# Kernel optimization log

Hardware: AMD Instinct MI355X
Metric: run time of the kernel (lower is better)

Reference implementation:

```python
import jax, jax.numpy as jnp
import numpy as np

C_Z = 128
C_S = 1024
C_S_OUT = 1024
B, L = 1, 1024


def setup_inputs() -> dict:
    key = jax.random.key(0)
    ks = jax.random.split(key, 8)
    s_z = jax.random.normal(ks[0], (B, L, L, C_Z), dtype=jnp.float32)
    s_s_in = jax.random.normal(ks[1], (B, L, C_S), dtype=jnp.float32)
    pair_mask = jnp.ones((B, L, L), dtype=jnp.float32)
    scale = 0.02
    return {
        "s_z": s_z,
        "s_s_in": s_s_in,
        "pair_mask": pair_mask,
        "ln_g": jnp.ones((C_Z,), jnp.float32),
        "ln_b": jnp.zeros((C_Z,), jnp.float32),
        "w1": jax.random.normal(ks[2], (C_Z, C_Z), jnp.float32) * scale,
        "b1": jnp.zeros((C_Z,), jnp.float32),
        "w2": jax.random.normal(ks[3], (C_Z, C_Z), jnp.float32) * scale,
        "b2": jnp.zeros((C_Z,), jnp.float32),
        "wc": jax.random.normal(ks[4], (C_S_OUT, 2 * C_Z + C_S), jnp.float32) * scale,
        "bc": jnp.zeros((C_S_OUT,), jnp.float32),
    }


def _layernorm(x, g, b, eps=1e-5):
    mu = jnp.mean(x, axis=-1, keepdims=True)
    var = jnp.mean(jnp.square(x - mu), axis=-1, keepdims=True)
    return (x - mu) * jax.lax.rsqrt(var + eps) * g + b


def reference(s_z, s_s_in, pair_mask, ln_g, ln_b, w1, b1, w2, b2, wc, bc):
    # LayerNorm -> Linear -> ReLU -> Linear over last dim (c_z)
    z = _layernorm(s_z, ln_g, ln_b)
    z = jax.nn.relu(jnp.einsum("blmc,dc->blmd", z, w1) + b1)
    z = jnp.einsum("blmc,dc->blmd", z, w2) + b2
    z = z * pair_mask[..., None]
    # masked mean over columns (dim=2) and rows (dim=1)
    norm_c = jnp.clip(jnp.sum(pair_mask, axis=2), 1.0, None)  # (B, L)
    s_s_c = jnp.sum(z, axis=2) / norm_c[..., None]            # (B, L, c_z)
    norm_r = jnp.clip(jnp.sum(pair_mask, axis=1), 1.0, None)
    s_s_r = jnp.sum(z, axis=1) / norm_r[..., None]
    cat = jnp.concatenate([s_s_c, s_s_r, s_s_in], axis=-1)    # (B, L, 2*c_z + c_s)
    return jnp.einsum("blc,dc->bld", cat, wc) + bc            # (B, L, c_s_out)
```

## Files before the change

### kernel.cpp

```cpp
#include <hip/hip_runtime.h>
#include <hip/hip_bf16.h>


typedef short bf16x8 __attribute__((ext_vector_type(8)));
typedef short short4v __attribute__((ext_vector_type(4)));
typedef float f32x16 __attribute__((ext_vector_type(16)));

static __device__ __forceinline__ short f2bf(float f) {
  unsigned u = __float_as_uint(f);
  u += 0x7fffu + ((u >> 16) & 1u);
  return (short)(u >> 16);
}
static __device__ __forceinline__ float bf2f(short s) {
  return __uint_as_float(((unsigned)(unsigned short)s) << 16);
}

__global__ __launch_bounds__(512, 4) void k_pair(
    const float* __restrict__ z, const float* __restrict__ pm,
    const float* __restrict__ lng, const float* __restrict__ lnb,
    const float* __restrict__ w1, const float* __restrict__ b1,
    float* __restrict__ gP, float* __restrict__ grP,
    float* __restrict__ Mc, float* __restrict__ Mr)
{
  __shared__ __align__(16) short As[2][64 * 136];
  __shared__ __align__(16) float rowdat[2][64][4];

  const int tid  = threadIdx.x;
  const int lane = tid & 63;
  const int wv   = tid >> 6;
  const int rt   = wv >> 2;
  const int cq   = wv & 3;
  const int ln   = lane & 31;
  const int hh   = lane >> 5;
  const int bx   = blockIdx.x, by = blockIdx.y;
  const int l0   = by * 32;
  const int m0   = bx * 32;
  const int c8   = (tid & 15) * 8;
  const int rstage = tid >> 4;

  const int dcol = cq * 32 + ln;
  float uacc = 0.f, wacc = 0.f;
  bf16x8 bF[8];
  #pragma unroll
  for (int k0 = 0; k0 < 8; ++k0) {
    const int kb = k0 * 16 + hh * 8;
    const float* wp = w1 + dcol * 128 + kb;
    float4 f0 = *(const float4*)wp;
    float4 f1 = *(const float4*)(wp + 4);
    float4 g0 = *(const float4*)(lng + kb);
    float4 g1 = *(const float4*)(lng + kb + 4);
    float4 e0 = *(const float4*)(lnb + kb);
    float4 e1 = *(const float4*)(lnb + kb + 4);
    float wr[8] = {f0.x, f0.y, f0.z, f0.w, f1.x, f1.y, f1.z, f1.w};
    float gg[8] = {g0.x, g0.y, g0.z, g0.w, g1.x, g1.y, g1.z, g1.w};
    float be[8] = {e0.x, e0.y, e0.z, e0.w, e1.x, e1.y, e1.z, e1.w};
    bf16x8 t;
    #pragma unroll
    for (int j = 0; j < 8; ++j) {
      t[j] = f2bf(wr[j] * gg[j]);
      uacc += bf2f(t[j]);
      wacc += wr[j] * be[j];
    }
    bF[k0] = t;
  }
  uacc += __shfl_xor(uacc, 32);
  wacc += __shfl_xor(wacc, 32);
  const float u_d  = uacc;
  const float wb_d = wacc + b1[dcol];

  float grA[16];
  #pragma unroll
  for (int i = 0; i < 16; ++i) grA[i] = 0.f;
  float mrAcc = 0.f;

  float4 xa[2], xb[2];
  float  mv = 0.f;
  auto LOADB = [&](int b) {
    #pragma unroll
    for (int p = 0; p < 2; ++p) {
      const int r = p * 32 + rstage;
      const int l = l0 + b * 2 + (r >> 5);
      const int m = m0 + (r & 31);
      const float* src = z + ((size_t)l * 1024 + (size_t)m) * 128 + c8;
      xa[p] = *(const float4*)src;
      xb[p] = *(const float4*)(src + 4);
    }
    if (tid < 64)
      mv = pm[(size_t)(l0 + b * 2 + (tid >> 5)) * 1024 + (m0 + (tid & 31))];
  };

  LOADB(0);

  #pragma unroll 1
  for (int b = 0; b < 16; ++b) {
    const int buf = b & 1;
    #pragma unroll
    for (int p = 0; p < 2; ++p) {
      const int r = p * 32 + rstage;
      float x[8] = {xa[p].x, xa[p].y, xa[p].z, xa[p].w,
                    xb[p].x, xb[p].y, xb[p].z, xb[p].w};
      float s = 0.f, s2 = 0.f;
      #pragma unroll
      for (int j = 0; j < 8; ++j) { s += x[j]; s2 = fmaf(x[j], x[j], s2); }
      #pragma unroll
      for (int off = 1; off < 16; off <<= 1) {
        s  += __shfl_xor(s, off);
        s2 += __shfl_xor(s2, off);
      }
      const float mu  = s * (1.f / 128.f);
      const float var = s2 * (1.f / 128.f) - mu * mu;
      const float rs  = rsqrtf(var + 1e-5f);
      bf16x8 o;
      #pragma unroll
      for (int j = 0; j < 8; ++j) o[j] = f2bf(x[j]);
      *(bf16x8*)(&As[buf][r * 136 + c8]) = o;
      if ((tid & 15) == 0) {
        rowdat[buf][r][0] = rs;
        rowdat[buf][r][1] = rs * mu;
      }
    }
    if (tid < 64) rowdat[buf][tid][2] = mv;
    __syncthreads();

    if (b < 15) LOADB(b + 1);

    f32x16 acc;
    #pragma unroll
    for (int i = 0; i < 16; ++i) acc[i] = 0.f;
    #pragma unroll
    for (int k0 = 0; k0 < 8; ++k0) {
      bf16x8 aF = *(bf16x8*)(&As[buf][(rt * 32 + ln) * 136 + k0 * 16 + hh * 8]);
      acc = __builtin_amdgcn_mfma_f32_32x32x16_bf16(aF, bF[k0], acc, 0, 0, 0);
    }

    const int lrow = l0 + b * 2 + rt;
    float s = 0.f;
    #pragma unroll
    for (int i = 0; i < 16; ++i) {
      const int cr = (i & 3) + 8 * (i >> 2) + 4 * hh;
      const float4 rd = *(const float4*)&rowdat[buf][rt * 32 + cr][0];
      const float h = fmaf(rd.x, acc[i], fmaf(-rd.y, u_d, wb_d));
      const float v = fmaxf(h, 0.f) * rd.z;
      grA[i] += v; s += v;
    }
    s += __shfl_xor(s, 32);
    if (lane < 32)
      gP[((size_t)bx * 1024 + lrow) * 128 + cq * 32 + lane] = s;

    if (wv == 0) {
      const float v = rowdat[buf][lane][2];
      mrAcc += v;
      float rsum = v;
      #pragma unroll
      for (int off = 1; off < 32; off <<= 1) rsum += __shfl_xor(rsum, off);
      if (ln == 0) atomicAdd(&Mc[l0 + b * 2 + hh], rsum);
    }
  }

  if (wv == 0) {
    const float v = mrAcc + __shfl_xor(mrAcc, 32);
    if (lane < 32) atomicAdd(&Mr[m0 + lane], v);
  }

  __syncthreads();
  float* red = (float*)&As[0][0];
  if (rt == 1) {
    #pragma unroll
    for (int i = 0; i < 16; ++i) {
      const int cr = (i & 3) + 8 * (i >> 2) + 4 * hh;
      red[(cq * 32 + cr) * 32 + ln] = grA[i];
    }
  }
  __syncthreads();
  if (rt == 0) {
    #pragma unroll
    for (int i = 0; i < 16; ++i) {
      const int cr = (i & 3) + 8 * (i >> 2) + 4 * hh;
      const float v = grA[i] + red[(cq * 32 + cr) * 32 + ln];
      grP[((size_t)by * 1024 + (m0 + cr)) * 128 + cq * 32 + ln] = v;
    }
  }
}

__global__ void k_reduce(const float* __restrict__ gP, const float* __restrict__ grP,
                         float* __restrict__ g, float* __restrict__ gr)
{
  const int idx = blockIdx.x * 256 + threadIdx.x;
  const bool isG = idx < 32768;
  const int t = isG ? idx : idx - 32768;
  const float* src = isG ? gP : grP;
  float* dst = isG ? g : gr;
  const int row = t >> 5;
  const int c4  = (t & 31) * 4;
  float4 s = {0.f, 0.f, 0.f, 0.f};
  #pragma unroll 8
  for (int x = 0; x < 32; ++x) {
    float4 v = *(const float4*)(src + ((size_t)x * 1024 + row) * 128 + c4);
    s.x += v.x; s.y += v.y; s.z += v.z; s.w += v.w;
  }
  *(float4*)(dst + (size_t)row * 128 + c4) = s;
}

__global__ __launch_bounds__(256, 2) void k_seqproj(
    const float* __restrict__ gg, const float* __restrict__ w2,
    const float* __restrict__ b2, const float* __restrict__ Mc,
    const float* __restrict__ Mr, short* __restrict__ Ah, short* __restrict__ Al)
{
  __shared__ __align__(16) short As[64 * 136];
  __shared__ float Mvs[64];

  const int tid = threadIdx.x, lane = tid & 63, wv = tid >> 6;
  const int rt = wv >> 1, ch = wv & 1, ln = lane & 31, hh = lane >> 5;
  const int r0 = blockIdx.x * 64;
  const int c8 = (tid & 15) * 8;

  float b2v[2];
  #pragma unroll
  for (int cc = 0; cc < 2; ++cc) b2v[cc] = b2[(ch * 2 + cc) * 32 + ln];

  bf16x8 bF[2][8];
  #pragma unroll
  for (int cc = 0; cc < 2; ++cc) {
    const int n = (ch * 2 + cc) * 32 + ln;
    #pragma unroll
    for (int k0 = 0; k0 < 8; ++k0) {
      const float* wp = w2 + n * 128 + k0 * 16 + hh * 8;
      float4 f0 = *(const float4*)wp;
      float4 f1 = *(const float4*)(wp + 4);
      bf16x8 t;
      t[0]=f2bf(f0.x); t[1]=f2bf(f0.y); t[2]=f2bf(f0.z); t[3]=f2bf(f0.w);
      t[4]=f2bf(f1.x); t[5]=f2bf(f1.y); t[6]=f2bf(f1.z); t[7]=f2bf(f1.w);
      bF[cc][k0] = t;
    }
  }

  #pragma unroll
  for (int p = 0; p < 4; ++p) {
    const int r = p * 16 + (tid >> 4);
    const float* src = gg + (size_t)(r0 + r) * 128 + c8;
    float4 f0 = *(const float4*)src;
    float4 f1 = *(const float4*)(src + 4);
    bf16x8 o;
    o[0]=f2bf(f0.x); o[1]=f2bf(f0.y); o[2]=f2bf(f0.z); o[3]=f2bf(f0.w);
    o[4]=f2bf(f1.x); o[5]=f2bf(f1.y); o[6]=f2bf(f1.z); o[7]=f2bf(f1.w);
    *(bf16x8*)(&As[r * 136 + c8]) = o;
  }
  if (tid < 64) {
    const int p = r0 + tid;
    Mvs[tid] = (p < 1024) ? Mc[p] : Mr[p - 1024];
  }
  __syncthreads();

  f32x16 acc0, acc1;
  #pragma unroll
  for (int i = 0; i < 16; ++i) { acc0[i] = 0.f; acc1[i] = 0.f; }
  #pragma unroll
  for (int k0 = 0; k0 < 8; ++k0) {
    bf16x8 aF = *(bf16x8*)(&As[(rt * 32 + ln) * 136 + k0 * 16 + hh * 8]);
    acc0 = __builtin_amdgcn_mfma_f32_32x32x16_bf16(aF, bF[0][k0], acc0, 0, 0, 0);
    acc1 = __builtin_amdgcn_mfma_f32_32x32x16_bf16(aF, bF[1][k0], acc1, 0, 0, 0);
  }

  const int base = (r0 < 1024) ? 0 : 128;
  #pragma unroll
  for (int i = 0; i < 16; ++i) {
    const int cr = (i & 3) + 8 * (i >> 2) + 4 * hh;
    const int p = r0 + rt * 32 + cr;
    const int row = p & 1023;
    const float mvv = Mvs[rt * 32 + cr];
    const float dn = fmaxf(mvv, 1.f);
    const float v0 = (acc0[i] + b2v[0] * mvv) / dn;
    const float v1 = (acc1[i] + b2v[1] * mvv) / dn;
    const int c0 = base + (ch * 2 + 0) * 32 + ln;
    const int c1 = base + (ch * 2 + 1) * 32 + ln;
    const short h0 = f2bf(v0), h1 = f2bf(v1);
    Ah[(size_t)row * 1280 + c0] = h0;
    Al[(size_t)row * 1280 + c0] = f2bf(v0 - bf2f(h0));
    Ah[(size_t)row * 1280 + c1] = h1;
    Al[(size_t)row * 1280 + c1] = f2bf(v1 - bf2f(h1));
  }
}

__global__ void k_split(const float* __restrict__ s_in, const float* __restrict__ wc,
                        short* __restrict__ Ah, short* __restrict__ Al,
                        short* __restrict__ Bh, short* __restrict__ Bl)
{
  const int idx = blockIdx.x * 256 + threadIdx.x;

  if (idx < 262144) {
    const int row = idx >> 8;
    const int c4  = (idx & 255) * 4;
    float4 v = *(const float4*)(s_in + (size_t)row * 1024 + c4);
    float x[4] = {v.x, v.y, v.z, v.w};
    short4v hi, lo;
    #pragma unroll
    for (int j = 0; j < 4; ++j) {
      const short h = f2bf(x[j]);
      hi[j] = h; lo[j] = f2bf(x[j] - bf2f(h));
    }
    const size_t o = (size_t)row * 1280 + 256 + c4;
    *(short4v*)(Ah + o) = hi;
    *(short4v*)(Al + o) = lo;
  }
  if (idx < 327680) {
    const int row = idx / 320;
    const int c4  = (idx - row * 320) * 4;
    float4 v = *(const float4*)(wc + (size_t)row * 1280 + c4);
    float x[4] = {v.x, v.y, v.z, v.w};
    short4v hi, lo;
    #pragma unroll
    for (int j = 0; j < 4; ++j) {
      const short h = f2bf(x[j]);
      hi[j] = h; lo[j] = f2bf(x[j] - bf2f(h));
    }
    const size_t o = (size_t)row * 1280 + c4;
    *(short4v*)(Bh + o) = hi;
    *(short4v*)(Bl + o) = lo;
  }
}

__global__ __launch_bounds__(256, 2) void k_final(
    const short* __restrict__ Ah, const short* __restrict__ Al,
    const short* __restrict__ Bh, const short* __restrict__ Bl,
    const float* __restrict__ bc, float* __restrict__ out)
{
  __shared__ __align__(16) short sAh[64 * 40], sAl[64 * 40];
  __shared__ __align__(16) short sBh[64 * 40], sBl[64 * 40];
  const int tid = threadIdx.x, lane = tid & 63, wv = tid >> 6;
  const int mi = (wv >> 1) * 32, ni = (wv & 1) * 32;
  const int ln = lane & 31, hh = lane >> 5;
  const int m0 = blockIdx.y * 64, n0 = blockIdx.x * 64;
  const int rS = tid >> 2;
  const int kb = (tid & 3) * 8;

  const float bcv = bc[n0 + ni + ln];
  f32x16 acc;
  #pragma unroll
  for (int i = 0; i < 16; ++i) acc[i] = 0.f;

  bf16x8 rAh, rAl, rBh, rBl;
  auto LOADK = [&](int kk0) {
    rAh = *(const bf16x8*)(Ah + (size_t)(m0 + rS) * 1280 + kk0 + kb);
    rAl = *(const bf16x8*)(Al + (size_t)(m0 + rS) * 1280 + kk0 + kb);
    rBh = *(const bf16x8*)(Bh + (size_t)(n0 + rS) * 1280 + kk0 + kb);
    rBl = *(const bf16x8*)(Bl + (size_t)(n0 + rS) * 1280 + kk0 + kb);
  };
  LOADK(0);

  #pragma unroll 1
  for (int kk0 = 0; kk0 < 1280; kk0 += 32) {
    if (kk0) __syncthreads();
    *(bf16x8*)(sAh + rS * 40 + kb) = rAh;
    *(bf16x8*)(sAl + rS * 40 + kb) = rAl;
    *(bf16x8*)(sBh + rS * 40 + kb) = rBh;
    *(bf16x8*)(sBl + rS * 40 + kb) = rBl;
    __syncthreads();
    if (kk0 < 1280 - 32) LOADK(kk0 + 32);

    #pragma unroll
    for (int k0 = 0; k0 < 2; ++k0) {
      bf16x8 aH = *(bf16x8*)(sAh + (mi + ln) * 40 + k0 * 16 + hh * 8);
      bf16x8 aL = *(bf16x8*)(sAl + (mi + ln) * 40 + k0 * 16 + hh * 8);
      bf16x8 bH = *(bf16x8*)(sBh + (ni + ln) * 40 + k0 * 16 + hh * 8);
      bf16x8 bL = *(bf16x8*)(sBl + (ni + ln) * 40 + k0 * 16 + hh * 8);
      acc = __builtin_amdgcn_mfma_f32_32x32x16_bf16(aH, bH, acc, 0, 0, 0);
      acc = __builtin_amdgcn_mfma_f32_32x32x16_bf16(aH, bL, acc, 0, 0, 0);
      acc = __builtin_amdgcn_mfma_f32_32x32x16_bf16(aL, bH, acc, 0, 0, 0);
    }
  }

  #pragma unroll
  for (int i = 0; i < 16; ++i) {
    const int cr = (i & 3) + 8 * (i >> 2) + 4 * hh;
    out[(size_t)(m0 + mi + cr) * 1024 + n0 + ni + ln] = acc[i] + bcv;
  }
}

extern "C" void kernel_launch(void* const* d_in, const int* in_sizes, int n_in,
                              void* d_out, int out_size, void* d_ws, size_t ws_size,
                              hipStream_t stream) {
  const float* s_z    = (const float*)d_in[0];
  const float* s_s_in = (const float*)d_in[1];
  const float* pmask  = (const float*)d_in[2];
  const float* ln_g   = (const float*)d_in[3];
  const float* ln_b   = (const float*)d_in[4];
  const float* w1     = (const float*)d_in[5];
  const float* b1     = (const float*)d_in[6];
  const float* w2     = (const float*)d_in[7];
  const float* b2     = (const float*)d_in[8];
  const float* wc     = (const float*)d_in[9];
  const float* bc     = (const float*)d_in[10];
  float* outp = (float*)d_out;

  float* Mc  = (float*)d_ws;
  float* Mr  = Mc + 1024;
  float* g   = Mr + 1024;
  float* gr  = g  + 131072;
  float* gP  = gr + 131072;
  float* grP = gP + 4194304;
  short* Ah  = (short*)(grP + 4194304);
  short* Al  = Ah + (size_t)1024 * 1280;
  short* Bh  = Al + (size_t)1024 * 1280;
  short* Bl  = Bh + (size_t)1024 * 1280;

  hipMemsetAsync(d_ws, 0, 2048 * sizeof(float), stream);

  k_split<<<1280, 256, 0, stream>>>(s_s_in, wc, Ah, Al, Bh, Bl);
  k_pair<<<dim3(32, 32), 512, 0, stream>>>(s_z, pmask, ln_g, ln_b, w1, b1, gP, grP, Mc, Mr);
  k_reduce<<<256, 256, 0, stream>>>(gP, grP, g, gr);
  k_seqproj<<<32, 256, 0, stream>>>(g, w2, b2, Mc, Mr, Ah, Al);
  k_final<<<dim3(16, 16), 256, 0, stream>>>(Ah, Al, Bh, Bl, bc, outp);
}
```

Baseline: 785.1 us.

## Replace partial-sum buffers with atomics, merge split into seqproj, double-buffer final GEMM

The pair kernel now atomically accumulates row and column sums straight into g/gr instead of writing 32-way partial buffers, so the k_reduce kernel and its 32 MB of partial traffic go away. The s_z loads become nontemporal so the streamed input does not pollute cache. The bf16 hi/lo split of s_s_in and wc is folded into the seqproj kernel as extra blocks, and k_final gains double-buffered LDS with a two-deep register prefetch. The costs are more float atomics (contention and nondeterministic summation order) and a larger memset.

```diff
diff --git a/kernel.cpp b/kernel.cpp
--- a/kernel.cpp
+++ b/kernel.cpp
@@ -5,6 +5,7 @@
 typedef short bf16x8 __attribute__((ext_vector_type(8)));
 typedef short short4v __attribute__((ext_vector_type(4)));
 typedef float f32x16 __attribute__((ext_vector_type(16)));
+typedef float f32x4 __attribute__((ext_vector_type(4)));
 
 static __device__ __forceinline__ short f2bf(float f) {
   unsigned u = __float_as_uint(f);
@@ -14,12 +15,15 @@
 static __device__ __forceinline__ float bf2f(short s) {
   return __uint_as_float(((unsigned)(unsigned short)s) << 16);
 }
+static __device__ __forceinline__ f32x4 ntload4(const float* p) {
+  return __builtin_nontemporal_load((const f32x4*)p);
+}
 
 __global__ __launch_bounds__(512, 4) void k_pair(
     const float* __restrict__ z, const float* __restrict__ pm,
     const float* __restrict__ lng, const float* __restrict__ lnb,
     const float* __restrict__ w1, const float* __restrict__ b1,
-    float* __restrict__ gP, float* __restrict__ grP,
+    float* __restrict__ g, float* __restrict__ gr,
     float* __restrict__ Mc, float* __restrict__ Mr)
 {
   __shared__ __align__(16) short As[2][64 * 136];
@@ -73,8 +77,8 @@
   for (int i = 0; i < 16; ++i) grA[i] = 0.f;
   float mrAcc = 0.f;
 
-  float4 xa[2], xb[2];
-  float  mv = 0.f;
+  f32x4 xa[2], xb[2];
+  float mv = 0.f;
   auto LOADB = [&](int b) {
     #pragma unroll
     for (int p = 0; p < 2; ++p) {
@@ -82,8 +86,8 @@
       const int l = l0 + b * 2 + (r >> 5);
       const int m = m0 + (r & 31);
       const float* src = z + ((size_t)l * 1024 + (size_t)m) * 128 + c8;
-      xa[p] = *(const float4*)src;
-      xb[p] = *(const float4*)(src + 4);
+      xa[p] = ntload4(src);
+      xb[p] = ntload4(src + 4);
     }
     if (tid < 64)
       mv = pm[(size_t)(l0 + b * 2 + (tid >> 5)) * 1024 + (m0 + (tid & 31))];
@@ -97,8 +101,8 @@
     #pragma unroll
     for (int p = 0; p < 2; ++p) {
       const int r = p * 32 + rstage;
-      float x[8] = {xa[p].x, xa[p].y, xa[p].z, xa[p].w,
-                    xb[p].x, xb[p].y, xb[p].z, xb[p].w};
+      float x[8] = {xa[p][0], xa[p][1], xa[p][2], xa[p][3],
+                    xb[p][0], xb[p][1], xb[p][2], xb[p][3]};
       float s = 0.f, s2 = 0.f;
       #pragma unroll
       for (int j = 0; j < 8; ++j) { s += x[j]; s2 = fmaf(x[j], x[j], s2); }
@@ -145,7 +149,7 @@
     }
     s += __shfl_xor(s, 32);
     if (lane < 32)
-      gP[((size_t)bx * 1024 + lrow) * 128 + cq * 32 + lane] = s;
+      atomicAdd(&g[lrow * 128 + cq * 32 + lane], s);
 
     if (wv == 0) {
       const float v = rowdat[buf][lane][2];
@@ -177,39 +181,60 @@
     for (int i = 0; i < 16; ++i) {
       const int cr = (i & 3) + 8 * (i >> 2) + 4 * hh;
       const float v = grA[i] + red[(cq * 32 + cr) * 32 + ln];
-      grP[((size_t)by * 1024 + (m0 + cr)) * 128 + cq * 32 + ln] = v;
-    }
-  }
-}
-
-__global__ void k_reduce(const float* __restrict__ gP, const float* __restrict__ grP,
-                         float* __restrict__ g, float* __restrict__ gr)
-{
-  const int idx = blockIdx.x * 256 + threadIdx.x;
-  const bool isG = idx < 32768;
-  const int t = isG ? idx : idx - 32768;
-  const float* src = isG ? gP : grP;
-  float* dst = isG ? g : gr;
-  const int row = t >> 5;
-  const int c4  = (t & 31) * 4;
-  float4 s = {0.f, 0.f, 0.f, 0.f};
-  #pragma unroll 8
-  for (int x = 0; x < 32; ++x) {
-    float4 v = *(const float4*)(src + ((size_t)x * 1024 + row) * 128 + c4);
-    s.x += v.x; s.y += v.y; s.z += v.z; s.w += v.w;
-  }
-  *(float4*)(dst + (size_t)row * 128 + c4) = s;
-}
-
-__global__ __launch_bounds__(256, 2) void k_seqproj(
+      atomicAdd(&gr[(m0 + cr) * 128 + cq * 32 + ln], v);
+    }
+  }
+}
+
+__global__ __launch_bounds__(256, 2) void k_seqsplit(
     const float* __restrict__ gg, const float* __restrict__ w2,
     const float* __restrict__ b2, const float* __restrict__ Mc,
-    const float* __restrict__ Mr, short* __restrict__ Ah, short* __restrict__ Al)
+    const float* __restrict__ Mr,
+    const float* __restrict__ s_in, const float* __restrict__ wc,
+    short* __restrict__ Ah, short* __restrict__ Al,
+    short* __restrict__ Bh, short* __restrict__ Bl)
 {
   __shared__ __align__(16) short As[64 * 136];
   __shared__ float Mvs[64];
 
-  const int tid = threadIdx.x, lane = tid & 63, wv = tid >> 6;
+  const int tid = threadIdx.x;
+
+  if (blockIdx.x >= 32) {
+    const int idx = (blockIdx.x - 32) * 256 + tid;
+    if (idx < 262144) {
+      const int row = idx >> 8;
+      const int c4  = (idx & 255) * 4;
+      float4 v = *(const float4*)(s_in + (size_t)row * 1024 + c4);
+      float x[4] = {v.x, v.y, v.z, v.w};
+      short4v hi, lo;
+      #pragma unroll
+      for (int j = 0; j < 4; ++j) {
+        const short h = f2bf(x[j]);
+        hi[j] = h; lo[j] = f2bf(x[j] - bf2f(h));
+      }
+      const size_t o = (size_t)row * 1280 + 256 + c4;
+      *(short4v*)(Ah + o) = hi;
+      *(short4v*)(Al + o) = lo;
+    }
+    if (idx < 327680) {
+      const int row = idx / 320;
+      const int c4  = (idx - row * 320) * 4;
+      float4 v = *(const float4*)(wc + (size_t)row * 1280 + c4);
+      float x[4] = {v.x, v.y, v.z, v.w};
+      short4v hi, lo;
+      #pragma unroll
+      for (int j = 0; j < 4; ++j) {
+        const short h = f2bf(x[j]);
+        hi[j] = h; lo[j] = f2bf(x[j] - bf2f(h));
+      }
+      const size_t o = (size_t)row * 1280 + c4;
+      *(short4v*)(Bh + o) = hi;
+      *(short4v*)(Bl + o) = lo;
+    }
+    return;
+  }
+
+  const int lane = tid & 63, wv = tid >> 6;
   const int rt = wv >> 1, ch = wv & 1, ln = lane & 31, hh = lane >> 5;
   const int r0 = blockIdx.x * 64;
   const int c8 = (tid & 15) * 8;
@@ -281,51 +306,13 @@
   }
 }
 
-__global__ void k_split(const float* __restrict__ s_in, const float* __restrict__ wc,
-                        short* __restrict__ Ah, short* __restrict__ Al,
-                        short* __restrict__ Bh, short* __restrict__ Bl)
-{
-  const int idx = blockIdx.x * 256 + threadIdx.x;
-
-  if (idx < 262144) {
-    const int row = idx >> 8;
-    const int c4  = (idx & 255) * 4;
-    float4 v = *(const float4*)(s_in + (size_t)row * 1024 + c4);
-    float x[4] = {v.x, v.y, v.z, v.w};
-    short4v hi, lo;
-    #pragma unroll
-    for (int j = 0; j < 4; ++j) {
-      const short h = f2bf(x[j]);
-      hi[j] = h; lo[j] = f2bf(x[j] - bf2f(h));
-    }
-    const size_t o = (size_t)row * 1280 + 256 + c4;
-    *(short4v*)(Ah + o) = hi;
-    *(short4v*)(Al + o) = lo;
-  }
-  if (idx < 327680) {
-    const int row = idx / 320;
-    const int c4  = (idx - row * 320) * 4;
-    float4 v = *(const float4*)(wc + (size_t)row * 1280 + c4);
-    float x[4] = {v.x, v.y, v.z, v.w};
-    short4v hi, lo;
-    #pragma unroll
-    for (int j = 0; j < 4; ++j) {
-      const short h = f2bf(x[j]);
-      hi[j] = h; lo[j] = f2bf(x[j] - bf2f(h));
-    }
-    const size_t o = (size_t)row * 1280 + c4;
-    *(short4v*)(Bh + o) = hi;
-    *(short4v*)(Bl + o) = lo;
-  }
-}
-
 __global__ __launch_bounds__(256, 2) void k_final(
     const short* __restrict__ Ah, const short* __restrict__ Al,
     const short* __restrict__ Bh, const short* __restrict__ Bl,
     const float* __restrict__ bc, float* __restrict__ out)
 {
-  __shared__ __align__(16) short sAh[64 * 40], sAl[64 * 40];
-  __shared__ __align__(16) short sBh[64 * 40], sBl[64 * 40];
+  __shared__ __align__(16) short sAh[2][64 * 40], sAl[2][64 * 40];
+  __shared__ __align__(16) short sBh[2][64 * 40], sBl[2][64 * 40];
   const int tid = threadIdx.x, lane = tid & 63, wv = tid >> 6;
   const int mi = (wv >> 1) * 32, ni = (wv & 1) * 32;
   const int ln = lane & 31, hh = lane >> 5;
@@ -338,31 +325,35 @@
   #pragma unroll
   for (int i = 0; i < 16; ++i) acc[i] = 0.f;
 
-  bf16x8 rAh, rAl, rBh, rBl;
-  auto LOADK = [&](int kk0) {
-    rAh = *(const bf16x8*)(Ah + (size_t)(m0 + rS) * 1280 + kk0 + kb);
-    rAl = *(const bf16x8*)(Al + (size_t)(m0 + rS) * 1280 + kk0 + kb);
-    rBh = *(const bf16x8*)(Bh + (size_t)(n0 + rS) * 1280 + kk0 + kb);
-    rBl = *(const bf16x8*)(Bl + (size_t)(n0 + rS) * 1280 + kk0 + kb);
+  bf16x8 rAh[2], rAl[2], rBh[2], rBl[2];
+  auto LOADK = [&](int s, int kk0) {
+    if (kk0 < 1280) {
+      rAh[s] = *(const bf16x8*)(Ah + (size_t)(m0 + rS) * 1280 + kk0 + kb);
+      rAl[s] = *(const bf16x8*)(Al + (size_t)(m0 + rS) * 1280 + kk0 + kb);
+      rBh[s] = *(const bf16x8*)(Bh + (size_t)(n0 + rS) * 1280 + kk0 + kb);
+      rBl[s] = *(const bf16x8*)(Bl + (size_t)(n0 + rS) * 1280 + kk0 + kb);
+    }
   };
-  LOADK(0);
+  LOADK(0, 0);
+  LOADK(1, 32);
 
   #pragma unroll 1
-  for (int kk0 = 0; kk0 < 1280; kk0 += 32) {
-    if (kk0) __syncthreads();
-    *(bf16x8*)(sAh + rS * 40 + kb) = rAh;
-    *(bf16x8*)(sAl + rS * 40 + kb) = rAl;
-    *(bf16x8*)(sBh + rS * 40 + kb) = rBh;
-    *(bf16x8*)(sBl + rS * 40 + kb) = rBl;
+  for (int it = 0; it < 40; ++it) {
+    const int kk0 = it * 32;
+    const int buf = it & 1;
+    *(bf16x8*)(&sAh[buf][rS * 40 + kb]) = rAh[buf];
+    *(bf16x8*)(&sAl[buf][rS * 40 + kb]) = rAl[buf];
+    *(bf16x8*)(&sBh[buf][rS * 40 + kb]) = rBh[buf];
+    *(bf16x8*)(&sBl[buf][rS * 40 + kb]) = rBl[buf];
     __syncthreads();
-    if (kk0 < 1280 - 32) LOADK(kk0 + 32);
+    LOADK(buf, kk0 + 64);
 
     #pragma unroll
     for (int k0 = 0; k0 < 2; ++k0) {
-      bf16x8 aH = *(bf16x8*)(sAh + (mi + ln) * 40 + k0 * 16 + hh * 8);
-      bf16x8 aL = *(bf16x8*)(sAl + (mi + ln) * 40 + k0 * 16 + hh * 8);
-      bf16x8 bH = *(bf16x8*)(sBh + (ni + ln) * 40 + k0 * 16 + hh * 8);
-      bf16x8 bL = *(bf16x8*)(sBl + (ni + ln) * 40 + k0 * 16 + hh * 8);
+      bf16x8 aH = *(bf16x8*)(&sAh[buf][(mi + ln) * 40 + k0 * 16 + hh * 8]);
+      bf16x8 aL = *(bf16x8*)(&sAl[buf][(mi + ln) * 40 + k0 * 16 + hh * 8]);
+      bf16x8 bH = *(bf16x8*)(&sBh[buf][(ni + ln) * 40 + k0 * 16 + hh * 8]);
+      bf16x8 bL = *(bf16x8*)(&sBl[buf][(ni + ln) * 40 + k0 * 16 + hh * 8]);
       acc = __builtin_amdgcn_mfma_f32_32x32x16_bf16(aH, bH, acc, 0, 0, 0);
       acc = __builtin_amdgcn_mfma_f32_32x32x16_bf16(aH, bL, acc, 0, 0, 0);
       acc = __builtin_amdgcn_mfma_f32_32x32x16_bf16(aL, bH, acc, 0, 0, 0);
@@ -396,18 +387,14 @@
   float* Mr  = Mc + 1024;
   float* g   = Mr + 1024;
   float* gr  = g  + 131072;
-  float* gP  = gr + 131072;
-  float* grP = gP + 4194304;
-  short* Ah  = (short*)(grP + 4194304);
+  short* Ah  = (short*)(gr + 131072);
   short* Al  = Ah + (size_t)1024 * 1280;
   short* Bh  = Al + (size_t)1024 * 1280;
   short* Bl  = Bh + (size_t)1024 * 1280;
 
-  hipMemsetAsync(d_ws, 0, 2048 * sizeof(float), stream);
-
-  k_split<<<1280, 256, 0, stream>>>(s_s_in, wc, Ah, Al, Bh, Bl);
-  k_pair<<<dim3(32, 32), 512, 0, stream>>>(s_z, pmask, ln_g, ln_b, w1, b1, gP, grP, Mc, Mr);
-  k_reduce<<<256, 256, 0, stream>>>(gP, grP, g, gr);
-  k_seqproj<<<32, 256, 0, stream>>>(g, w2, b2, Mc, Mr, Ah, Al);
+  hipMemsetAsync(d_ws, 0, (size_t)(2048 + 262144) * sizeof(float), stream);
+
+  k_pair<<<dim3(32, 32), 512, 0, stream>>>(s_z, pmask, ln_g, ln_b, w1, b1, g, gr, Mc, Mr);
+  k_seqsplit<<<1312, 256, 0, stream>>>(g, w2, b2, Mc, Mr, s_s_in, wc, Ah, Al, Bh, Bl);
   k_final<<<dim3(16, 16), 256, 0, stream>>>(Ah, Al, Bh, Bl, bc, outp);
 }
```

Result: slower. 890.8 us (+13.5%).
